# Kernel optimization log

Hardware: AMD Instinct MI355X
Metric: run time of the kernel (lower is better)

## Reference

```python
import jax, jax.numpy as jnp
import numpy as np

DIM, NH, T_MAX = 1024, 16, 2048
HD = DIM // NH
EPS = 1e-6


def _rope_tables(T, hd, dtype=jnp.float32):
    inv_freq = 1.0 / (10000.0 ** (jnp.arange(0, hd, 2, dtype=jnp.float32) / hd))
    t = jnp.arange(T, dtype=jnp.float32)
    freqs = jnp.outer(t, inv_freq)                 # [T, hd/2]
    emb = jnp.concatenate([freqs, freqs], axis=-1)  # [T, hd]
    return jnp.cos(emb).astype(dtype), jnp.sin(emb).astype(dtype)


def _rotate_half(x):
    x1, x2 = jnp.split(x, 2, axis=-1)
    return jnp.concatenate([-x2, x1], axis=-1)


def _rmsnorm(x, g):
    rms = jnp.sqrt(jnp.mean(x * x, axis=-1, keepdims=True) + EPS)
    return x / rms * g


def setup_inputs() -> dict:
    key = jax.random.key(0)
    ks = jax.random.split(key, 10)
    B, T, C = 4, 2048, DIM
    s = 1.0 / np.sqrt(C)
    x = jax.random.normal(ks[0], (B, T, C), dtype=jnp.float32)
    mask = jnp.tril(jnp.ones((T, T), dtype=jnp.int32))[None, None, :, :]
    wq = jax.random.normal(ks[1], (C, C), jnp.float32) * s
    wk = jax.random.normal(ks[2], (C, C), jnp.float32) * s
    wv = jax.random.normal(ks[3], (C, C), jnp.float32) * s
    wo = jax.random.normal(ks[4], (C, C), jnp.float32) * s
    w1 = jax.random.normal(ks[5], (C, 4 * C), jnp.float32) * s
    w2 = jax.random.normal(ks[6], (4 * C, C), jnp.float32) * (1.0 / np.sqrt(4 * C))
    w3 = jax.random.normal(ks[7], (C, 4 * C), jnp.float32) * s
    g1 = jnp.ones((C,), jnp.float32)
    g2 = jnp.ones((C,), jnp.float32)
    return {"x": x, "mask": mask, "g1": g1, "wq": wq, "wk": wk, "wv": wv,
            "wo": wo, "g2": g2, "w1": w1, "w2": w2, "w3": w3}


def reference(x, mask, g1, wq, wk, wv, wo, g2, w1, w2, w3):
    B, T, C = x.shape
    scale = HD ** -0.5
    # --- attention sublayer ---
    h = _rmsnorm(x, g1)
    q = (h @ wq).reshape(B, T, NH, HD)
    k = (h @ wk).reshape(B, T, NH, HD)
    v = (h @ wv).reshape(B, T, NH, HD)
    cos, sin = _rope_tables(T, HD, x.dtype)
    cos = cos[None, :, None, :]
    sin = sin[None, :, None, :]
    q = q * cos + _rotate_half(q) * sin
    k = k * cos + _rotate_half(k) * sin
    attn = jnp.einsum("bthd,bshd->bhts", q, k) * scale  # [B,H,T,T]
    attn = jnp.where(mask == 0, -jnp.inf, attn)
    attn = jax.nn.softmax(attn, axis=-1)
    o = jnp.einsum("bhts,bshd->bthd", attn, v).reshape(B, T, C)
    x = x + o @ wo
    # --- SwiGLU FFN sublayer ---
    h = _rmsnorm(x, g2)
    x = x + (jax.nn.silu(h @ w1) * (h @ w3)) @ w2
    return x
```

## Files before the change

kernel.cpp:

```cpp
#include <hip/hip_runtime.h>
#include <cstdint>

typedef unsigned short u16;
typedef __attribute__((ext_vector_type(8))) short bf16x8;
typedef __attribute__((ext_vector_type(4))) float f32x4;

__device__ __forceinline__ u16 f2b(float f) {
  union { float f; unsigned u; } c; c.f = f;
  unsigned u = c.u;
  return (u16)((u + 0x7FFFu + ((u >> 16) & 1u)) >> 16);
}
__device__ __forceinline__ float b2f(u16 b) {
  union { unsigned u; float f; } c; c.u = ((unsigned)b) << 16;
  return c.f;
}

typedef __attribute__((address_space(1))) void gv_t;
typedef __attribute__((address_space(3))) void lv_t;
__device__ __forceinline__ void gload_lds16(const void* g, void* l) {
  __builtin_amdgcn_global_load_lds((gv_t*)g, (lv_t*)l, 16, 0, 0);
}

__global__ void transpose_f2b(const float* __restrict__ in, u16* __restrict__ out,
                              int R, int C) {
  __shared__ float t[32][33];
  const int c0 = blockIdx.x * 32, r0 = blockIdx.y * 32;
  const int tx = threadIdx.x, ty = threadIdx.y;
#pragma unroll
  for (int i = 0; i < 4; ++i)
    t[ty + 8 * i][tx] = in[(size_t)(r0 + ty + 8 * i) * C + c0 + tx];
  __syncthreads();
#pragma unroll
  for (int i = 0; i < 4; ++i)
    out[(size_t)(c0 + ty + 8 * i) * R + r0 + tx] = f2b(t[tx][ty + 8 * i]);
}

__global__ __launch_bounds__(256) void rmsnorm_k(const float* __restrict__ x,
                                                 const float* __restrict__ g,
                                                 u16* __restrict__ out) {
  const int row = blockIdx.x, tid = threadIdx.x;
  const float4 v = ((const float4*)x)[(size_t)row * 256 + tid];
  float ss = v.x * v.x + v.y * v.y + v.z * v.z + v.w * v.w;
#pragma unroll
  for (int off = 1; off < 64; off <<= 1) ss += __shfl_xor(ss, off, 64);
  __shared__ float red[4];
  if ((tid & 63) == 0) red[tid >> 6] = ss;
  __syncthreads();
  const float mean = (red[0] + red[1] + red[2] + red[3]) * (1.0f / 1024.0f);
  const float rinv = 1.0f / sqrtf(mean + 1e-6f);
  const float4 gv = ((const float4*)g)[tid];
  u16* o = out + (size_t)row * 1024 + tid * 4;
  o[0] = f2b(v.x * rinv * gv.x);
  o[1] = f2b(v.y * rinv * gv.y);
  o[2] = f2b(v.z * rinv * gv.z);
  o[3] = f2b(v.w * rinv * gv.w);
}

__global__ __launch_bounds__(256) void rope_k(u16* __restrict__ qkv) {
  const int i = blockIdx.x * 256 + threadIdx.x;
  const int d = i & 31;
  const int h = (i >> 5) & 15;
  const int bt = i >> 9;
  const int t = bt & 2047;
  const float inv = exp2f((float)d * -0.4152410118609203f);
  const float th = (float)t * inv;
  float s, c;
  sincosf(th, &s, &c);
  size_t base = (size_t)bt * 3072 + h * 64 + d;
#pragma unroll
  for (int half = 0; half < 2; ++half) {
    const float x1 = b2f(qkv[base]);
    const float x2 = b2f(qkv[base + 32]);
    qkv[base]      = f2b(x1 * c - x2 * s);
    qkv[base + 32] = f2b(x2 * c + x1 * s);
    base += 1024;
  }
}

__global__ void vtrans_k(const u16* __restrict__ qkv, u16* __restrict__ VT) {
  __shared__ u16 tl[32][34];
  const int t0 = blockIdx.x * 32;
  const int bh = blockIdx.y >> 1;
  const int d0 = (blockIdx.y & 1) * 32;
  const int b = bh >> 4, h = bh & 15;
  const int tx = threadIdx.x, ty = threadIdx.y;
  const u16* src = qkv + (size_t)(b * 2048 + t0) * 3072 + 2048 + h * 64 + d0;
#pragma unroll
  for (int i = 0; i < 4; ++i)
    tl[ty + 8 * i][tx] = src[(size_t)(ty + 8 * i) * 3072 + tx];
  __syncthreads();
  u16* dst = VT + ((size_t)bh * 64 + d0) * 2048 + t0;
#pragma unroll
  for (int i = 0; i < 4; ++i)
    dst[(size_t)(ty + 8 * i) * 2048 + tx] = tl[tx][ty + 8 * i];
}

template <int EPI>
__global__ __launch_bounds__(256)
void gemm_bt(const u16* __restrict__ A, const u16* __restrict__ BT,
             void* __restrict__ Cout, const float* __restrict__ resid,
             int M, int N, int K, int lda) {
  __shared__ alignas(16) u16 As[128 * 32];
  __shared__ alignas(16) u16 Bs[128 * 32];
  const int tid = threadIdx.x;
  const int wave = tid >> 6, lane = tid & 63;
  const int wr = wave >> 1, wc = wave & 1;
  const int l15 = lane & 15, quad = lane >> 4;
  const int bm = blockIdx.x * 128, bn = blockIdx.y * 128;

  f32x4 acc[4][4];
#pragma unroll
  for (int i = 0; i < 4; ++i)
#pragma unroll
    for (int j = 0; j < 4; ++j) acc[i][j] = (f32x4){0.f, 0.f, 0.f, 0.f};

  const int srow = wave * 32 + (lane >> 2);
  const int scol = (lane & 3) * 8;
  const u16* gA0 = A + (size_t)(bm + srow) * lda + scol;
  const u16* gA1 = gA0 + (size_t)16 * lda;
  const u16* gB0 = BT + (size_t)(bn + srow) * K + scol;
  const u16* gB1 = gB0 + (size_t)16 * K;
  u16* lA0 = As + wave * 1024; u16* lA1 = lA0 + 512;
  u16* lB0 = Bs + wave * 1024; u16* lB1 = lB0 + 512;

  const u16* pa = As + (wr * 64 + l15) * 32 + quad * 8;
  const u16* pb = Bs + (wc * 64 + l15) * 32 + quad * 8;

  for (int kt = 0; kt < K; kt += 32) {
    gload_lds16(gA0 + kt, lA0);
    gload_lds16(gA1 + kt, lA1);
    gload_lds16(gB0 + kt, lB0);
    gload_lds16(gB1 + kt, lB1);
    __syncthreads();
    bf16x8 af[4], bfv[4];
#pragma unroll
    for (int i = 0; i < 4; ++i) af[i] = *(const bf16x8*)(pa + i * 512);
#pragma unroll
    for (int j = 0; j < 4; ++j) bfv[j] = *(const bf16x8*)(pb + j * 512);
#pragma unroll
    for (int i = 0; i < 4; ++i)
#pragma unroll
      for (int j = 0; j < 4; ++j)
        acc[i][j] = __builtin_amdgcn_mfma_f32_16x16x32_bf16(af[i], bfv[j], acc[i][j], 0, 0, 0);
    __syncthreads();
  }

#pragma unroll
  for (int i = 0; i < 4; ++i) {
    const int gr = bm + wr * 64 + i * 16 + quad * 4;
#pragma unroll
    for (int j = 0; j < 4; ++j) {
      const int gc = bn + wc * 64 + j * 16 + l15;
#pragma unroll
      for (int r = 0; r < 4; ++r) {
        const size_t off = (size_t)(gr + r) * N + gc;
        if (EPI == 0) {
          ((u16*)Cout)[off] = f2b(acc[i][j][r]);
        } else {
          ((float*)Cout)[off] = resid[off] + acc[i][j][r];
        }
      }
    }
  }
}

template <int EPI>
__global__ __launch_bounds__(512, 2)
void gemm256(const u16* __restrict__ A, const u16* __restrict__ BT,
             void* __restrict__ Cout, const float* __restrict__ resid,
             int M, int N, int K, int lda) {
  __shared__ alignas(16) u16 LDS[65536];
  char* const ldsc = (char*)LDS;
  const int tid = threadIdx.x;
  const int wave = tid >> 6, lane = tid & 63;
  const int wr = wave >> 2, wc = wave & 3;
  const int l15 = lane & 15, quad = lane >> 4;
  const int bm = blockIdx.x * 256, bn = blockIdx.y * 256;
  const int NT = K >> 6;
  const int NIT = NT >> 1;

  const int swz = (l15 & 8) << 2;
  const int aoff = (((wr * 64 + l15) * 64 + quad * 16) ^ swz);
  const int boff = (((wc * 32 + l15) * 64 + quad * 16) ^ swz) + 65536;

  const int kperm = ((lane & 3) ^ ((lane >> 5) << 1)) * 8;
  const u16* sA = A + (size_t)(bm + wave * 16 + (lane >> 2)) * lda + kperm;
  const u16* sB = BT + (size_t)(bn + wave * 16 + (lane >> 2)) * K + kperm;
  const size_t hA = (size_t)128 * lda;
  const size_t hB = (size_t)128 * K;
  const int dstW = wave * 1024;

  f32x4 acc[8][4];
#pragma unroll
  for (int m = 0; m < 8; ++m)
#pragma unroll
    for (int n = 0; n < 4; ++n) acc[m][n] = (f32x4){0.f, 0.f, 0.f, 0.f};
  bf16x8 a[4][2], b[2][2];

#define STAGE(kt_, slot_, buf_)                                               \
  if ((kt_) < NT) {                                                           \
    const u16* s_ = (((slot_) & 1) ? sB + ((size_t)((slot_) >> 1)) * hB       \
                                   : sA + ((size_t)((slot_) >> 1)) * hA) +    \
                    (size_t)(kt_) * 64;                                       \
    char* d_ = ldsc + (((slot_) & 1) ? 65536 : 0) + (buf_) * 32768 +          \
               ((slot_) >> 1) * 16384 + dstW;                                 \
    gload_lds16(s_, d_);                                                      \
    gload_lds16(s_ + 32, d_ + 8192);                                          \
  }

#define LOAD_A(mh_, buf_)                                                     \
  _Pragma("unroll") for (int mf = 0; mf < 4; ++mf)                            \
      _Pragma("unroll") for (int kk = 0; kk < 2; ++kk)                        \
          a[mf][kk] = *(const bf16x8*)(ldsc + aoff + (buf_) * 32768 +         \
                                       (mh_) * 16384 + kk * 8192 + mf * 1024);

#define LOAD_B(nh_, buf_)                                                     \
  _Pragma("unroll") for (int nf = 0; nf < 2; ++nf)                            \
      _Pragma("unroll") for (int kk = 0; kk < 2; ++kk)                        \
          b[nf][kk] = *(const bf16x8*)(ldsc + boff + (buf_) * 32768 +         \
                                       (nh_) * 16384 + kk * 8192 + nf * 1024);

#define MMA(mh_, nh_)                                                         \
  __builtin_amdgcn_s_setprio(1);                                              \
  _Pragma("unroll") for (int mf = 0; mf < 4; ++mf)                            \
      _Pragma("unroll") for (int nf = 0; nf < 2; ++nf)                        \
          _Pragma("unroll") for (int kk = 0; kk < 2; ++kk)                    \
              acc[(mh_) * 4 + mf][(nh_) * 2 + nf] =                           \
                  __builtin_amdgcn_mfma_f32_16x16x32_bf16(                    \
                      a[mf][kk], b[nf][kk],                                   \
                      acc[(mh_) * 4 + mf][(nh_) * 2 + nf], 0, 0, 0);          \
  __builtin_amdgcn_s_setprio(0);

#define BAR() __builtin_amdgcn_s_barrier()
#define DRAIN_LGKM()                                                          \
  {                                                                           \
    asm volatile("s_waitcnt lgkmcnt(0)" ::: "memory");                        \
    __builtin_amdgcn_sched_barrier(0);                                        \
  }

  STAGE(0, 0, 0); STAGE(0, 1, 0); STAGE(0, 2, 0); STAGE(0, 3, 0);
  STAGE(1, 0, 1); STAGE(1, 1, 1);
  asm volatile("s_waitcnt vmcnt(4)" ::: "memory");
  BAR();

  for (int i = 0; i < NIT; ++i) {
    const int t = 2 * i;
    LOAD_A(0, 0); LOAD_B(0, 0); STAGE(t + 1, 2, 1);
    BAR(); DRAIN_LGKM(); MMA(0, 0); BAR();
    LOAD_B(1, 0); STAGE(t + 1, 3, 1);
    BAR(); DRAIN_LGKM(); MMA(0, 1); BAR();
    LOAD_A(1, 0); LOAD_B(0, 0); STAGE(t + 2, 0, 0);
    BAR(); DRAIN_LGKM(); MMA(1, 0); BAR();
    LOAD_B(1, 0); STAGE(t + 2, 1, 0);
    BAR(); DRAIN_LGKM(); MMA(1, 1);
    if (i == NIT - 1) { asm volatile("s_waitcnt vmcnt(0)" ::: "memory"); }
    else              { asm volatile("s_waitcnt vmcnt(4)" ::: "memory"); }
    BAR();
    LOAD_A(0, 1); LOAD_B(0, 1); STAGE(t + 2, 2, 0);
    BAR(); DRAIN_LGKM(); MMA(0, 0); BAR();
    LOAD_B(1, 1); STAGE(t + 2, 3, 0);
    BAR(); DRAIN_LGKM(); MMA(0, 1); BAR();
    LOAD_A(1, 1); LOAD_B(0, 1); STAGE(t + 3, 0, 1);
    BAR(); DRAIN_LGKM(); MMA(1, 0); BAR();
    LOAD_B(1, 1); STAGE(t + 3, 1, 1);
    BAR(); DRAIN_LGKM(); MMA(1, 1);
    if (i < NIT - 1) { asm volatile("s_waitcnt vmcnt(4)" ::: "memory"); }
    BAR();
  }
#undef STAGE
#undef LOAD_A
#undef LOAD_B
#undef MMA

#pragma unroll
  for (int m = 0; m < 8; ++m) {
    const int gr = bm + (m >> 2) * 128 + wr * 64 + (m & 3) * 16 + quad * 4;
#pragma unroll
    for (int n = 0; n < 4; ++n) {
      const int gc = bn + (n >> 1) * 128 + wc * 32 + (n & 1) * 16 + l15;
#pragma unroll
      for (int r = 0; r < 4; ++r) {
        const size_t off = (size_t)(gr + r) * N + gc;
        if (EPI == 0) {
          ((u16*)Cout)[off] = f2b(acc[m][n][r]);
        } else {
          ((float*)Cout)[off] = resid[off] + acc[m][n][r];
        }
      }
    }
  }
#undef BAR
#undef DRAIN_LGKM
}

template <int EPI>
__global__ __launch_bounds__(512, 2)
void gemm256n(const u16* __restrict__ A, const u16* __restrict__ BT,
              void* __restrict__ Cout, const float* __restrict__ resid,
              int M, int N, int K, int lda) {
  __shared__ alignas(16) u16 LDS[49152];
  char* const ldsc = (char*)LDS;
  const int tid = threadIdx.x;
  const int wave = tid >> 6, lane = tid & 63;
  const int wr = wave >> 2, wc = wave & 3;
  const int l15 = lane & 15, quad = lane >> 4;
  const int bm = blockIdx.x * 256, bn = blockIdx.y * 128;
  const int NT = K >> 6;

  const int swz = (l15 & 8) << 2;
  const int aoff = (((wr * 64 + l15) * 64 + quad * 16) ^ swz);
  const int boff = (((wc * 32 + l15) * 64 + quad * 16) ^ swz) + 65536;

  const int kperm = ((lane & 3) ^ ((lane >> 5) << 1)) * 8;
  const u16* sA = A + (size_t)(bm + wave * 16 + (lane >> 2)) * lda + kperm;
  const u16* sB = BT + (size_t)(bn + wave * 16 + (lane >> 2)) * K + kperm;
  const size_t hA = (size_t)128 * lda;
  const int dstW = wave * 1024;

  f32x4 acc[8][2];
#pragma unroll
  for (int m = 0; m < 8; ++m)
#pragma unroll
    for (int n = 0; n < 2; ++n) acc[m][n] = (f32x4){0.f, 0.f, 0.f, 0.f};
  bf16x8 a[4][2], b[2][2];

#define STAGE_A(kt_, half_, buf_)                                             \
  if ((kt_) < NT) {                                                           \
    const u16* s_ = sA + (size_t)(half_) * hA + (size_t)(kt_) * 64;           \
    char* d_ = ldsc + (buf_) * 32768 + (half_) * 16384 + dstW;                \
    gload_lds16(s_, d_);                                                      \
    gload_lds16(s_ + 32, d_ + 8192);                                          \
  }
#define STAGE_B(kt_, buf_)                                                    \
  if ((kt_) < NT) {                                                           \
    const u16* s_ = sB + (size_t)(kt_) * 64;                                  \
    char* d_ = ldsc + 65536 + (buf_) * 16384 + dstW;                          \
    gload_lds16(s_, d_);                                                      \
    gload_lds16(s_ + 32, d_ + 8192);                                          \
  }
#define LOAD_A(mh_, buf_)                                                     \
  _Pragma("unroll") for (int mf = 0; mf < 4; ++mf)                            \
      _Pragma("unroll") for (int kk = 0; kk < 2; ++kk)                        \
          a[mf][kk] = *(const bf16x8*)(ldsc + aoff + (buf_) * 32768 +         \
                                       (mh_) * 16384 + kk * 8192 + mf * 1024);
#define LOAD_B(buf_)                                                          \
  _Pragma("unroll") for (int nf = 0; nf < 2; ++nf)                            \
      _Pragma("unroll") for (int kk = 0; kk < 2; ++kk)                        \
          b[nf][kk] = *(const bf16x8*)(ldsc + boff + (buf_) * 16384 +         \
                                       kk * 8192 + nf * 1024);
#define MMA(mh_)                                                              \
  __builtin_amdgcn_s_setprio(1);                                              \
  _Pragma("unroll") for (int mf = 0; mf < 4; ++mf)                            \
      _Pragma("unroll") for (int nf = 0; nf < 2; ++nf)                        \
          _Pragma("unroll") for (int kk = 0; kk < 2; ++kk)                    \
              acc[(mh_) * 4 + mf][nf] =                                       \
                  __builtin_amdgcn_mfma_f32_16x16x32_bf16(                    \
                      a[mf][kk], b[nf][kk], acc[(mh_) * 4 + mf][nf], 0, 0, 0);\
  __builtin_amdgcn_s_setprio(0);
#define BAR() __builtin_amdgcn_s_barrier()
#define DRAIN_LGKM()                                                          \
  {                                                                           \
    asm volatile("s_waitcnt lgkmcnt(0)" ::: "memory");                        \
    __builtin_amdgcn_sched_barrier(0);                                        \
  }

  STAGE_A(0, 0, 0); STAGE_B(0, 0);
  STAGE_A(0, 1, 0);
  STAGE_A(1, 0, 1); STAGE_B(1, 1);
  asm volatile("s_waitcnt vmcnt(6)" ::: "memory");
  BAR();

  for (int t = 0; t < NT; ++t) {
    const int bsel = t & 1;
    LOAD_A(0, bsel); LOAD_B(bsel);
    STAGE_A(t + 1, 1, bsel ^ 1);
    BAR(); DRAIN_LGKM(); MMA(0);
    if (t == NT - 1) { asm volatile("s_waitcnt vmcnt(0)" ::: "memory"); }
    else             { asm volatile("s_waitcnt vmcnt(6)" ::: "memory"); }
    BAR();
    LOAD_A(1, bsel);
    STAGE_A(t + 2, 0, bsel); STAGE_B(t + 2, bsel);
    BAR(); DRAIN_LGKM(); MMA(1);
    if (t == NT - 2)     { asm volatile("s_waitcnt vmcnt(2)" ::: "memory"); }
    else if (t < NT - 2) { asm volatile("s_waitcnt vmcnt(6)" ::: "memory"); }
    BAR();
  }
#undef STAGE_A
#undef STAGE_B
#undef LOAD_A
#undef LOAD_B
#undef MMA
#undef BAR
#undef DRAIN_LGKM

#pragma unroll
  for (int m = 0; m < 8; ++m) {
    const int gr = bm + (m >> 2) * 128 + wr * 64 + (m & 3) * 16 + quad * 4;
#pragma unroll
    for (int n = 0; n < 2; ++n) {
      const int gc = bn + wc * 32 + n * 16 + l15;
#pragma unroll
      for (int r = 0; r < 4; ++r) {
        const size_t off = (size_t)(gr + r) * N + gc;
        if (EPI == 0) {
          ((u16*)Cout)[off] = f2b(acc[m][n][r]);
        } else {
          ((float*)Cout)[off] = resid[off] + acc[m][n][r];
        }
      }
    }
  }
}

__global__ __launch_bounds__(256)
void attn_kernel(const u16* __restrict__ QKV, const u16* __restrict__ VT,
                 u16* __restrict__ O) {
  const int T = 2048, stQ = 3072;
  const int tid = threadIdx.x, wave = tid >> 6, lane = tid & 63;
  const int l15 = lane & 15, quad = lane >> 4;
  const int qt = (int)gridDim.x - 1 - (int)blockIdx.x;
  const int qb0 = qt * 128;
  const int bh = blockIdx.y, b = bh >> 4, h = bh & 15;
  const float sc2 = 0.125f * 1.44269504088896f;
  const float M0 = 32.0f;

  __shared__ alignas(16) u16 Kf[2][8 * 512];
  __shared__ alignas(16) u16 Vf[2][8 * 512];
  __shared__ alignas(16) u16 Pl[4][2][16 * 72];

  const u16* Qb  = QKV + (size_t)b * T * stQ + h * 64;
  const u16* Kb  = Qb + 1024;
  const u16* VTb = VT + (size_t)bh * 64 * T;

  const int r0 = qb0 + wave * 16;
  const int r1 = r0 + 64;
  const u16* qp0 = Qb + (size_t)(r0 + l15) * stQ + quad * 8;
  const u16* qp1 = Qb + (size_t)(r1 + l15) * stQ + quad * 8;
  const bf16x8 qf00 = *(const bf16x8*)qp0;
  const bf16x8 qf01 = *(const bf16x8*)(qp0 + 32);
  const bf16x8 qf10 = *(const bf16x8*)qp1;
  const bf16x8 qf11 = *(const bf16x8*)(qp1 + 32);

  bf16x8 ones;
#pragma unroll
  for (int j = 0; j < 8; ++j) ones[j] = (short)0x3F80;

  const u16* kS = Kb + (size_t)(wave * 16 + l15) * stQ + quad * 8;
  const u16* vS = VTb + (size_t)(wave * 16 + l15) * T + quad * 8;

  f32x4 o0[4], o1[4], sum0, sum1;
#pragma unroll
  for (int c = 0; c < 4; ++c) {
    o0[c] = (f32x4){0.f, 0.f, 0.f, 0.f};
    o1[c] = (f32x4){0.f, 0.f, 0.f, 0.f};
  }
  sum0 = (f32x4){0.f, 0.f, 0.f, 0.f};
  sum1 = (f32x4){0.f, 0.f, 0.f, 0.f};

  u16* pw0 = &Pl[wave][0][0];
  u16* pw1 = &Pl[wave][1][0];

  const int nkt = qt * 2 + 2;

  gload_lds16(kS,      &Kf[0][(wave * 2 + 0) * 512]);
  gload_lds16(kS + 32, &Kf[0][(wave * 2 + 1) * 512]);
  gload_lds16(vS,      &Vf[0][(wave * 2 + 0) * 512]);
  gload_lds16(vS + 32, &Vf[0][(wave * 2 + 1) * 512]);

  for (int kt = 0; kt < nkt; ++kt) {
    const int kb0 = kt * 64;
    const int buf = kt & 1;
    __builtin_amdgcn_sched_barrier(0);
    if (kt + 1 < nkt) {
      const size_t kb1 = (size_t)(kb0 + 64);
      gload_lds16(kS + kb1 * stQ,      &Kf[buf ^ 1][(wave * 2 + 0) * 512]);
      gload_lds16(kS + kb1 * stQ + 32, &Kf[buf ^ 1][(wave * 2 + 1) * 512]);
      gload_lds16(vS + kb1,            &Vf[buf ^ 1][(wave * 2 + 0) * 512]);
      gload_lds16(vS + kb1 + 32,       &Vf[buf ^ 1][(wave * 2 + 1) * 512]);
      asm volatile("s_waitcnt vmcnt(4)" ::: "memory");
    } else {
      asm volatile("s_waitcnt vmcnt(0)" ::: "memory");
    }
    __builtin_amdgcn_s_barrier();
    __builtin_amdgcn_sched_barrier(0);

    bf16x8 kf[8], vf[8];
#pragma unroll
    for (int g = 0; g < 8; ++g) {
      kf[g] = *(const bf16x8*)(&Kf[buf][g * 512 + lane * 8]);
      vf[g] = *(const bf16x8*)(&Vf[buf][g * 512 + lane * 8]);
    }

    const bool act0 = (kb0 <= r0 + 15);

    {
      f32x4 s[4];
      __builtin_amdgcn_s_setprio(1);
#pragma unroll
      for (int jj = 0; jj < 4; ++jj) {
        s[jj] = (f32x4){0.f, 0.f, 0.f, 0.f};
        s[jj] = __builtin_amdgcn_mfma_f32_16x16x32_bf16(qf10, kf[jj * 2 + 0], s[jj], 0, 0, 0);
        s[jj] = __builtin_amdgcn_mfma_f32_16x16x32_bf16(qf11, kf[jj * 2 + 1], s[jj], 0, 0, 0);
      }
      __builtin_amdgcn_s_setprio(0);
      if (kb0 + 63 > r1) {
#pragma unroll
        for (int jj = 0; jj < 4; ++jj)
#pragma unroll
          for (int r = 0; r < 4; ++r) {
            const bool msk = (kb0 + jj * 16 + l15) > (r1 + quad * 4 + r);
            const float a = msk ? -1e30f : (s[jj][r] * sc2 - M0);
            pw1[(quad * 4 + r) * 72 + jj * 16 + l15] = f2b(exp2f(a));
          }
      } else {
#pragma unroll
        for (int jj = 0; jj < 4; ++jj)
#pragma unroll
          for (int r = 0; r < 4; ++r)
            pw1[(quad * 4 + r) * 72 + jj * 16 + l15] =
                f2b(exp2f(s[jj][r] * sc2 - M0));
      }
    }
    if (act0) {
      f32x4 s[4];
      __builtin_amdgcn_s_setprio(1);
#pragma unroll
      for (int jj = 0; jj < 4; ++jj) {
        s[jj] = (f32x4){0.f, 0.f, 0.f, 0.f};
        s[jj] = __builtin_amdgcn_mfma_f32_16x16x32_bf16(qf00, kf[jj * 2 + 0], s[jj], 0, 0, 0);
        s[jj] = __builtin_amdgcn_mfma_f32_16x16x32_bf16(qf01, kf[jj * 2 + 1], s[jj], 0, 0, 0);
      }
      __builtin_amdgcn_s_setprio(0);
      if (kb0 + 63 > r0) {
#pragma unroll
        for (int jj = 0; jj < 4; ++jj)
#pragma unroll
          for (int r = 0; r < 4; ++r) {
            const bool msk = (kb0 + jj * 16 + l15) > (r0 + quad * 4 + r);
            const float a = msk ? -1e30f : (s[jj][r] * sc2 - M0);
            pw0[(quad * 4 + r) * 72 + jj * 16 + l15] = f2b(exp2f(a));
          }
      } else {
#pragma unroll
        for (int jj = 0; jj < 4; ++jj)
#pragma unroll
          for (int r = 0; r < 4; ++r)
            pw0[(quad * 4 + r) * 72 + jj * 16 + l15] =
                f2b(exp2f(s[jj][r] * sc2 - M0));
      }
    }

    const bf16x8 pf10 = *(const bf16x8*)(pw1 + l15 * 72 + quad * 8);
    const bf16x8 pf11 = *(const bf16x8*)(pw1 + l15 * 72 + 32 + quad * 8);
    __builtin_amdgcn_s_setprio(1);
#pragma unroll
    for (int c = 0; c < 4; ++c) {
      o1[c] = __builtin_amdgcn_mfma_f32_16x16x32_bf16(pf10, vf[c * 2 + 0], o1[c], 0, 0, 0);
      o1[c] = __builtin_amdgcn_mfma_f32_16x16x32_bf16(pf11, vf[c * 2 + 1], o1[c], 0, 0, 0);
    }
    sum1 = __builtin_amdgcn_mfma_f32_16x16x32_bf16(pf10, ones, sum1, 0, 0, 0);
    sum1 = __builtin_amdgcn_mfma_f32_16x16x32_bf16(pf11, ones, sum1, 0, 0, 0);
    __builtin_amdgcn_s_setprio(0);
    if (act0) {
      const bf16x8 pf00 = *(const bf16x8*)(pw0 + l15 * 72 + quad * 8);
      const bf16x8 pf01 = *(const bf16x8*)(pw0 + l15 * 72 + 32 + quad * 8);
      __builtin_amdgcn_s_setprio(1);
#pragma unroll
      for (int c = 0; c < 4; ++c) {
        o0[c] = __builtin_amdgcn_mfma_f32_16x16x32_bf16(pf00, vf[c * 2 + 0], o0[c], 0, 0, 0);
        o0[c] = __builtin_amdgcn_mfma_f32_16x16x32_bf16(pf01, vf[c * 2 + 1], o0[c], 0, 0, 0);
      }
      sum0 = __builtin_amdgcn_mfma_f32_16x16x32_bf16(pf00, ones, sum0, 0, 0, 0);
      sum0 = __builtin_amdgcn_mfma_f32_16x16x32_bf16(pf01, ones, sum0, 0, 0, 0);
      __builtin_amdgcn_s_setprio(0);
    }
    __builtin_amdgcn_s_barrier();
  }

  float i0[4], i1[4];
#pragma unroll
  for (int r = 0; r < 4; ++r) { i0[r] = 1.f / sum0[r]; i1[r] = 1.f / sum1[r]; }
  u16* op0 = O + ((size_t)(b * T) + r0 + quad * 4) * 1024 + h * 64 + l15;
  u16* op1 = O + ((size_t)(b * T) + r1 + quad * 4) * 1024 + h * 64 + l15;
#pragma unroll
  for (int c = 0; c < 4; ++c)
#pragma unroll
    for (int r = 0; r < 4; ++r) {
      op0[(size_t)r * 1024 + c * 16] = f2b(o0[c][r] * i0[r]);
      op1[(size_t)r * 1024 + c * 16] = f2b(o1[c][r] * i1[r]);
    }
}

__global__ __launch_bounds__(256) void gate_k(u16* __restrict__ a13) {
  const size_t i = (size_t)blockIdx.x * 256 + threadIdx.x;
  const size_t row = i >> 9, c8 = (i & 511) * 8;
  u16* p1v = a13 + row * 8192 + c8;
  const u16* p3v = p1v + 4096;
  uint4 u1 = *(uint4*)p1v;
  const uint4 u3 = *(const uint4*)p3v;
  u16* p1 = (u16*)&u1;
  const u16* p3 = (const u16*)&u3;
#pragma unroll
  for (int j = 0; j < 8; ++j) {
    const float a = b2f(p1[j]);
    const float g = b2f(p3[j]);
    const float s = a / (1.f + __expf(-a));
    p1[j] = f2b(s * g);
  }
  *(uint4*)p1v = u1;
}

extern "C" void kernel_launch(void* const* d_in, const int* in_sizes, int n_in,
                              void* d_out, int out_size, void* d_ws, size_t ws_size,
                              hipStream_t stream) {
  const float* x  = (const float*)d_in[0];
  const float* g1 = (const float*)d_in[2];
  const float* wq = (const float*)d_in[3];
  const float* wk = (const float*)d_in[4];
  const float* wv = (const float*)d_in[5];
  const float* wo = (const float*)d_in[6];
  const float* g2 = (const float*)d_in[7];
  const float* w1 = (const float*)d_in[8];
  const float* w2 = (const float*)d_in[9];
  const float* w3 = (const float*)d_in[10];
  float* out = (float*)d_out;

  const int T = 2048, NH = 16, B = 4;
  const int M = B * T;
  const size_t MB = 1ull << 20;

  char* ws = (char*)d_ws;
  u16* hb    = (u16*)(ws);
  u16* wqkvT = (u16*)(ws + 16 * MB);
  u16* woT   = (u16*)(ws + 22 * MB);
  u16* w13T  = (u16*)(ws + 24 * MB);
  u16* w2T   = (u16*)(ws + 40 * MB);
  u16* qkv   = (u16*)(ws + 48 * MB);
  u16* VT    = (u16*)(ws + 96 * MB);
  u16* Ob    = (u16*)(ws + 112 * MB);
  u16* a13   = (u16*)(ws + 48 * MB);

  const dim3 tb(32, 8);
  transpose_f2b<<<dim3(32, 32),  tb, 0, stream>>>(wq, wqkvT,              1024, 1024);
  transpose_f2b<<<dim3(32, 32),  tb, 0, stream>>>(wk, wqkvT + 1024*1024,  1024, 1024);
  transpose_f2b<<<dim3(32, 32),  tb, 0, stream>>>(wv, wqkvT + 2048*1024,  1024, 1024);
  transpose_f2b<<<dim3(32, 32),  tb, 0, stream>>>(wo, woT, 1024, 1024);
  transpose_f2b<<<dim3(128, 32), tb, 0, stream>>>(w1, w13T,               1024, 4096);
  transpose_f2b<<<dim3(128, 32), tb, 0, stream>>>(w3, w13T + 4096*1024,   1024, 4096);
  transpose_f2b<<<dim3(32, 128), tb, 0, stream>>>(w2, w2T, 4096, 1024);

  rmsnorm_k<<<M, 256, 0, stream>>>(x, g1, hb);

  gemm256<0><<<dim3(32, 12), 512, 0, stream>>>(hb, wqkvT, qkv, nullptr, M, 3072, 1024, 1024);

  rope_k<<<16384, 256, 0, stream>>>(qkv);
  vtrans_k<<<dim3(64, 128), tb, 0, stream>>>(qkv, VT);

  attn_kernel<<<dim3(T / 128, B * NH), 256, 0, stream>>>(qkv, VT, Ob);

  gemm256n<1><<<dim3(32, 8), 512, 0, stream>>>(Ob, woT, out, x, M, 1024, 1024, 1024);

  rmsnorm_k<<<M, 256, 0, stream>>>(out, g2, hb);

  gemm256<0><<<dim3(32, 32), 512, 0, stream>>>(hb, w13T, a13, nullptr, M, 8192, 1024, 1024);

  gate_k<<<16384, 256, 0, stream>>>(a13);

  gemm256n<1><<<dim3(32, 8), 512, 0, stream>>>(a13, w2T, out, out, M, 1024, 4096, 8192);
}
```

Measured before the change: 693.5 us.

## Split long causal attention query tiles across two blocks and combine partials

Query tiles 5-15 of the causal attention are now split into two key-range chunks handled by separate blocks. Each chunk writes unnormalized fp32 partial outputs and row sums to a workspace, and a new combine kernel adds them and normalizes. The grid grows from 16 to 27 blocks per head so the long diagonal tiles stop dominating the tail and load balances better across CUs. This costs an extra kernel launch and fp32 partial traffic, and it relies on a fixed softmax max offset so the partials can be summed without rescaling.

```diff
diff --git a/kernel.cpp b/kernel.cpp
--- a/kernel.cpp
+++ b/kernel.cpp
@@ -414,11 +414,20 @@
 
 __global__ __launch_bounds__(256)
 void attn_kernel(const u16* __restrict__ QKV, const u16* __restrict__ VT,
-                 u16* __restrict__ O) {
+                 u16* __restrict__ O, float* __restrict__ Opart,
+                 float* __restrict__ Spart) {
   const int T = 2048, stQ = 3072;
   const int tid = threadIdx.x, wave = tid >> 6, lane = tid & 63;
   const int l15 = lane & 15, quad = lane >> 4;
-  const int qt = (int)gridDim.x - 1 - (int)blockIdx.x;
+
+  const int xi = (int)blockIdx.x;
+  const bool split = (xi < 22);
+  const int qt = split ? (15 - (xi >> 1)) : (26 - xi);
+  const int chunk = split ? (xi & 1) : 0;
+  const int len = split ? (qt + 1) : (2 * qt + 2);
+  const int kt0 = chunk * (qt + 1);
+  const int ktEnd = kt0 + len;
+
   const int qb0 = qt * 128;
   const int bh = blockIdx.y, b = bh >> 4, h = bh & 15;
   const float sc2 = 0.125f * 1.44269504088896f;
@@ -460,18 +469,16 @@
   u16* pw0 = &Pl[wave][0][0];
   u16* pw1 = &Pl[wave][1][0];
 
-  const int nkt = qt * 2 + 2;
-
-  gload_lds16(kS,      &Kf[0][(wave * 2 + 0) * 512]);
-  gload_lds16(kS + 32, &Kf[0][(wave * 2 + 1) * 512]);
-  gload_lds16(vS,      &Vf[0][(wave * 2 + 0) * 512]);
-  gload_lds16(vS + 32, &Vf[0][(wave * 2 + 1) * 512]);
-
-  for (int kt = 0; kt < nkt; ++kt) {
+  gload_lds16(kS + (size_t)(kt0 * 64) * stQ,      &Kf[0][(wave * 2 + 0) * 512]);
+  gload_lds16(kS + (size_t)(kt0 * 64) * stQ + 32, &Kf[0][(wave * 2 + 1) * 512]);
+  gload_lds16(vS + (size_t)(kt0 * 64),            &Vf[0][(wave * 2 + 0) * 512]);
+  gload_lds16(vS + (size_t)(kt0 * 64) + 32,       &Vf[0][(wave * 2 + 1) * 512]);
+
+  for (int kt = kt0; kt < ktEnd; ++kt) {
     const int kb0 = kt * 64;
-    const int buf = kt & 1;
+    const int buf = (kt - kt0) & 1;
     __builtin_amdgcn_sched_barrier(0);
-    if (kt + 1 < nkt) {
+    if (kt + 1 < ktEnd) {
       const size_t kb1 = (size_t)(kb0 + 64);
       gload_lds16(kS + kb1 * stQ,      &Kf[buf ^ 1][(wave * 2 + 0) * 512]);
       gload_lds16(kS + kb1 * stQ + 32, &Kf[buf ^ 1][(wave * 2 + 1) * 512]);
@@ -577,18 +584,64 @@
     __builtin_amdgcn_s_barrier();
   }
 
-  float i0[4], i1[4];
-#pragma unroll
-  for (int r = 0; r < 4; ++r) { i0[r] = 1.f / sum0[r]; i1[r] = 1.f / sum1[r]; }
-  u16* op0 = O + ((size_t)(b * T) + r0 + quad * 4) * 1024 + h * 64 + l15;
-  u16* op1 = O + ((size_t)(b * T) + r1 + quad * 4) * 1024 + h * 64 + l15;
-#pragma unroll
-  for (int c = 0; c < 4; ++c)
-#pragma unroll
-    for (int r = 0; r < 4; ++r) {
-      op0[(size_t)r * 1024 + c * 16] = f2b(o0[c][r] * i0[r]);
-      op1[(size_t)r * 1024 + c * 16] = f2b(o1[c][r] * i1[r]);
-    }
+  if (split) {
+    const int pi = (bh * 11 + (qt - 5)) * 2 + chunk;
+    float* Po = Opart + (size_t)pi * 8192;
+    float* Ps = Spart + (size_t)pi * 128;
+    const int lr0 = wave * 16 + quad * 4;
+#pragma unroll
+    for (int c = 0; c < 4; ++c)
+#pragma unroll
+      for (int r = 0; r < 4; ++r) {
+        Po[(lr0 + r) * 64 + c * 16 + l15]      = o0[c][r];
+        Po[(64 + lr0 + r) * 64 + c * 16 + l15] = o1[c][r];
+      }
+    if (l15 == 0) {
+#pragma unroll
+      for (int r = 0; r < 4; ++r) {
+        Ps[lr0 + r]      = sum0[r];
+        Ps[64 + lr0 + r] = sum1[r];
+      }
+    }
+  } else {
+    float i0[4], i1[4];
+#pragma unroll
+    for (int r = 0; r < 4; ++r) { i0[r] = 1.f / sum0[r]; i1[r] = 1.f / sum1[r]; }
+    u16* op0 = O + ((size_t)(b * T) + r0 + quad * 4) * 1024 + h * 64 + l15;
+    u16* op1 = O + ((size_t)(b * T) + r1 + quad * 4) * 1024 + h * 64 + l15;
+#pragma unroll
+    for (int c = 0; c < 4; ++c)
+#pragma unroll
+      for (int r = 0; r < 4; ++r) {
+        op0[(size_t)r * 1024 + c * 16] = f2b(o0[c][r] * i0[r]);
+        op1[(size_t)r * 1024 + c * 16] = f2b(o1[c][r] * i1[r]);
+      }
+  }
+}
+
+__global__ __launch_bounds__(256)
+void attn_combine(const float* __restrict__ Opart, const float* __restrict__ Spart,
+                  u16* __restrict__ O) {
+  const int sp = blockIdx.x;
+  const int bh = sp / 11, qt = 5 + (sp % 11);
+  const int b = bh >> 4, h = bh & 15;
+  const int t = threadIdx.x;
+  const int row = t >> 1, ch = (t & 1) * 32;
+  const size_t p0 = (size_t)(2 * sp) * 8192, p1 = p0 + 8192;
+  const float s = Spart[(size_t)(2 * sp) * 128 + row] +
+                  Spart[(size_t)(2 * sp) * 128 + 128 + row];
+  const float inv = 1.f / s;
+  const float4* A  = (const float4*)(Opart + p0 + row * 64 + ch);
+  const float4* Bv = (const float4*)(Opart + p1 + row * 64 + ch);
+  u16* op = O + ((size_t)(b * 2048) + qt * 128 + row) * 1024 + h * 64 + ch;
+#pragma unroll
+  for (int j = 0; j < 8; ++j) {
+    const float4 a = A[j], bb = Bv[j];
+    op[j * 4 + 0] = f2b((a.x + bb.x) * inv);
+    op[j * 4 + 1] = f2b((a.y + bb.y) * inv);
+    op[j * 4 + 2] = f2b((a.z + bb.z) * inv);
+    op[j * 4 + 3] = f2b((a.w + bb.w) * inv);
+  }
 }
 
 __global__ __launch_bounds__(256) void gate_k(u16* __restrict__ a13) {
@@ -639,6 +692,8 @@
   u16* VT    = (u16*)(ws + 96 * MB);
   u16* Ob    = (u16*)(ws + 112 * MB);
   u16* a13   = (u16*)(ws + 48 * MB);
+  float* Opart = (float*)(ws + 128 * MB);
+  float* Spart = Opart + (size_t)1408 * 8192;
 
   const dim3 tb(32, 8);
   transpose_f2b<<<dim3(32, 32),  tb, 0, stream>>>(wq, wqkvT,              1024, 1024);
@@ -656,7 +711,8 @@
   rope_k<<<16384, 256, 0, stream>>>(qkv);
   vtrans_k<<<dim3(64, 128), tb, 0, stream>>>(qkv, VT);
 
-  attn_kernel<<<dim3(T / 128, B * NH), 256, 0, stream>>>(qkv, VT, Ob);
+  attn_kernel<<<dim3(27, B * NH), 256, 0, stream>>>(qkv, VT, Ob, Opart, Spart);
+  attn_combine<<<dim3(704), 256, 0, stream>>>(Opart, Spart, Ob);
 
   gemm256n<1><<<dim3(32, 8), 512, 0, stream>>>(Ob, woT, out, x, M, 1024, 1024, 1024);
 
```

New measurement: 672.9 us. 1.03x faster.
